# Performance work log

Hardware: AMD Instinct MI355X
Metric: run time of the kernel (lower is better)

Reference implementation:

```python
import jax, jax.numpy as jnp
import numpy as np
from math import sqrt

BATCH = 32
NUM_CLASSES = 81   # incl. background (class 0 skipped)
MAX_DET = 200      # max_output / per-class NMS candidate cap
IOU_T = 0.5        # criteria in decode_batch_with_nms_trace
CONF_T = 0.05      # score mask threshold


def make_dboxes():
    """Replicates dboxes_R34_coco([1200,1200]) -> (15130, 4) xywh, clipped to [0,1]."""
    fig = 1200
    feat = [50, 25, 13, 7, 3, 3]
    scales = [int(s * fig / 300) for s in [21, 45, 99, 153, 207, 261, 315]]
    ars = [[2], [2, 3], [2, 3], [2, 3], [2], [2]]
    boxes = []
    for idx, f in enumerate(feat):
        sk1 = scales[idx] / fig
        sk2 = scales[idx + 1] / fig
        sk3 = sqrt(sk1 * sk2)
        sizes = [(sk1, sk1), (sk3, sk3)]
        for a in ars[idx]:
            w, h = sk1 * sqrt(a), sk1 / sqrt(a)
            sizes += [(w, h), (h, w)]
        fk = fig // (fig // f)
        for (w, h) in sizes:
            for i in range(f):
                for j in range(f):
                    boxes.append(((j + 0.5) / fk, (i + 0.5) / fk, w, h))
    return np.clip(np.asarray(boxes, np.float32), 0.0, 1.0)


def setup_inputs() -> dict:
    key = jax.random.key(0)
    k1, k2 = jax.random.split(key)
    db = make_dboxes()                      # (15130, 4)
    N = db.shape[0]
    return {
        "bboxes_in": jax.random.normal(k1, (BATCH, 4, N), jnp.float32),
        "scores_in": jax.random.normal(k2, (BATCH, NUM_CLASSES, N), jnp.float32),
        "scale_xy": jnp.full((1,), 0.1, jnp.float32),
        "scale_wh": jnp.full((1,), 0.2, jnp.float32),
        "dboxes_xywh": jnp.asarray(db)[None],  # (1, N, 4)
    }


def _scale_back(bboxes_in, scores_in, scale_xy, scale_wh, dboxes_xywh):
    bb = jnp.transpose(bboxes_in, (0, 2, 1))          # (B, N, 4)
    sc = jnp.transpose(scores_in, (0, 2, 1))          # (B, N, L)
    d_xy, d_wh = dboxes_xywh[..., :2], dboxes_xywh[..., 2:]
    xy = bb[..., :2] * scale_xy * d_wh + d_xy
    wh = jnp.exp(bb[..., 2:] * scale_wh) * d_wh
    ltrb = jnp.concatenate([xy - 0.5 * wh, xy + 0.5 * wh], axis=-1)
    return ltrb, jax.nn.softmax(sc, axis=-1)


def _pairwise_iou(a, b):
    lt = jnp.maximum(a[:, None, :2], b[None, :, :2])
    rb = jnp.minimum(a[:, None, 2:], b[None, :, 2:])
    wh = jnp.clip(rb - lt, 0.0)
    inter = wh[..., 0] * wh[..., 1]
    area_a = (a[:, 2] - a[:, 0]) * (a[:, 3] - a[:, 1])
    area_b = (b[:, 2] - b[:, 0]) * (b[:, 3] - b[:, 1])
    return inter / (area_a[:, None] + area_b[None, :] - inter)


def _nms_one_class(boxes, cls_scores):
    """boxes (N,4), cls_scores (N,) -> (MAX_DET,4), (MAX_DET,) with suppressed = -1."""
    s = jnp.where(cls_scores > CONF_T, cls_scores, -1.0)   # mask score > 0.05
    top_s, idx = jax.lax.top_k(s, MAX_DET)                 # descending topk
    b = boxes[idx]
    iou = _pairwise_iou(b, b)                              # (K, K)
    valid = top_s > CONF_T

    def body(i, keep):  # greedy NMS over score-sorted candidates
        sup = (iou[i] > IOU_T) & keep[i] & (jnp.arange(MAX_DET) > i)
        return keep & ~sup

    keep = jax.lax.stop_gradient(jax.lax.fori_loop(0, MAX_DET, body, valid))
    return b, jnp.where(keep, top_s, -1.0)


def _decode(bboxes_in, scores_in, scale_xy, scale_wh, dboxes_xywh):
    boxes, probs = _scale_back(bboxes_in, scores_in, scale_xy, scale_wh, dboxes_xywh)
    cls_scores = jnp.transpose(probs[..., 1:], (0, 2, 1))   # (B, C=80, N); skip bg
    B, C = cls_scores.shape[0], cls_scores.shape[1]
    per_class = jax.vmap(_nms_one_class, in_axes=(None, 0))
    kb, ks = jax.vmap(per_class, in_axes=(0, 0))(boxes, cls_scores)  # (B,C,K,4),(B,C,K)
    labels = jnp.broadcast_to(
        jnp.arange(1, C + 1, dtype=jnp.int32)[:, None], (C, MAX_DET)).reshape(-1)
    kb = kb.reshape(B, C * MAX_DET, 4)
    ks = ks.reshape(B, C * MAX_DET)
    top_s, top_i = jax.lax.top_k(ks, MAX_DET)               # global top-200
    fb = jnp.take_along_axis(kb, top_i[..., None], axis=1)  # (B, 200, 4)
    fl = labels[top_i]                                      # (B, 200)
    valid = top_s > CONF_T
    return (fb * valid[..., None].astype(fb.dtype),
            jnp.where(valid, fl, 0),
            jnp.where(valid, top_s, 0.0))


def reference(bboxes_in, scores_in, scale_xy, scale_wh, dboxes_xywh):
    return _decode(bboxes_in, scores_in, scale_xy, scale_wh, dboxes_xywh)
```

## Files before the change

### kernel.cpp

```cpp
#include <hip/hip_runtime.h>
#include <stdint.h>

#define NPRIOR   15130
#define BATCH    32
#define NCLS     81
#define NCLS_OUT 80
#define NDET     200
#define CONF_T   0.05f
#define IOU_T    0.5f
#define CAND_CAP 1024
#define NGRP     5
#define GRP      16

__global__ __launch_bounds__(256) void zero_counters(unsigned int* __restrict__ counters, int n) {
    int i = blockIdx.x * 256 + threadIdx.x;
    if (i < n) counters[i] = 0u;
}

__global__ __launch_bounds__(256) void decode_softmax_scatter(
    const float* __restrict__ bboxes,
    const float* __restrict__ scores,
    const float* __restrict__ scale_xy_p,
    const float* __restrict__ scale_wh_p,
    const float* __restrict__ dboxes,
    float* __restrict__ boxes_ltrb,
    unsigned int* __restrict__ counters,
    unsigned long long* __restrict__ cand_g)
{
    int b = blockIdx.y;
    int n = blockIdx.x * 256 + threadIdx.x;
    if (n >= NPRIOR) return;

    float sx = scale_xy_p[0], sw = scale_wh_p[0];
    const float* bb = bboxes + (size_t)b * 4 * NPRIOR + n;
    float bx = bb[0];
    float by = bb[NPRIOR];
    float bw = bb[2 * NPRIOR];
    float bh = bb[3 * NPRIOR];
    float dx = dboxes[n * 4 + 0], dy = dboxes[n * 4 + 1];
    float dw = dboxes[n * 4 + 2], dh = dboxes[n * 4 + 3];
    float x = __fadd_rn(__fmul_rn(__fmul_rn(bx, sx), dw), dx);
    float y = __fadd_rn(__fmul_rn(__fmul_rn(by, sx), dh), dy);
    float w = __fmul_rn(expf(__fmul_rn(bw, sw)), dw);
    float h = __fmul_rn(expf(__fmul_rn(bh, sw)), dh);
    float hw = __fmul_rn(0.5f, w), hh = __fmul_rn(0.5f, h);
    float4 box;
    box.x = __fsub_rn(x, hw);
    box.y = __fsub_rn(y, hh);
    box.z = __fadd_rn(x, hw);
    box.w = __fadd_rn(y, hh);
    ((float4*)boxes_ltrb)[(size_t)b * NPRIOR + n] = box;

    const float* sc = scores + (size_t)b * NCLS * NPRIOR + n;
    float v[NCLS];
    float mx = -INFINITY;
#pragma unroll
    for (int c = 0; c < NCLS; ++c) {
        v[c] = sc[(size_t)c * NPRIOR];
        mx = fmaxf(mx, v[c]);
    }
    float sum = 0.f;
#pragma unroll
    for (int c = 0; c < NCLS; ++c) {
        v[c] = expf(__fsub_rn(v[c], mx));
        sum = __fadd_rn(sum, v[c]);
    }

    unsigned int invn = 0xFFFFFFFFu - (unsigned int)n;
#pragma unroll
    for (int c = 1; c < NCLS; ++c) {
        float p = __fdiv_rn(v[c], sum);
        if (p > CONF_T) {
            unsigned int idx = (unsigned int)b * NCLS_OUT + (unsigned int)(c - 1);
            unsigned int pos = atomicAdd(&counters[idx], 1u);
            if (pos < CAND_CAP) {
                cand_g[(size_t)idx * CAND_CAP + pos] =
                    ((unsigned long long)__float_as_uint(p) << 32) | (unsigned long long)invn;
            }
        }
    }
}

__device__ inline void bitonic_desc(unsigned long long* keys, int P, int tid) {
    for (int k = 2; k <= P; k <<= 1) {
        for (int j = k >> 1; j > 0; j >>= 1) {
            for (int i = tid; i < P; i += 256) {
                int l = i ^ j;
                if (l > i) {
                    unsigned long long a = keys[i], b = keys[l];
                    bool desc = ((i & k) == 0);
                    if (desc ? (a < b) : (a > b)) {
                        keys[i] = b;
                        keys[l] = a;
                    }
                }
            }
            __syncthreads();
        }
    }
}

__global__ __launch_bounds__(256) void nms_class(
    const unsigned int* __restrict__ counters,
    const unsigned long long* __restrict__ cand_g,
    const float* __restrict__ boxes_ltrb,
    float* __restrict__ cls_scores,
    float* __restrict__ cls_boxes)
{
    __shared__ unsigned long long cand[CAND_CAP];
    __shared__ float sbox[NDET][4];
    __shared__ float sscore[NDET];
    __shared__ unsigned long long rowm[NDET][4];
    __shared__ unsigned long long keepw[4];

    int tid = threadIdx.x;
    int b = blockIdx.y;
    int bc = b * NCLS_OUT + blockIdx.x;

    unsigned int cntu = counters[bc];
    int cnt = (cntu > CAND_CAP) ? CAND_CAP : (int)cntu;

    int P = 256;
    while (P < cnt) P <<= 1;

    for (int i = tid; i < P; i += 256)
        cand[i] = (i < cnt) ? cand_g[(size_t)bc * CAND_CAP + i] : 0ull;
    __syncthreads();

    bitonic_desc(cand, P, tid);

    int m = cnt < NDET ? cnt : NDET;
    if (tid < m) {
        unsigned long long key = cand[tid];
        unsigned int n = 0xFFFFFFFFu - (unsigned int)(key & 0xFFFFFFFFull);
        sscore[tid] = __uint_as_float((unsigned int)(key >> 32));
        float4 bx = ((const float4*)boxes_ltrb)[(size_t)b * NPRIOR + n];
        sbox[tid][0] = bx.x;
        sbox[tid][1] = bx.y;
        sbox[tid][2] = bx.z;
        sbox[tid][3] = bx.w;
    }
    __syncthreads();

    if (tid < m) {
        float l0 = sbox[tid][0], t0 = sbox[tid][1], r0 = sbox[tid][2], b0 = sbox[tid][3];
        float area0 = __fmul_rn(__fsub_rn(r0, l0), __fsub_rn(b0, t0));
        unsigned long long w0 = 0, w1 = 0, w2 = 0, w3 = 0;
        for (int j = tid + 1; j < m; ++j) {
            float lj = sbox[j][0], tj = sbox[j][1], rj = sbox[j][2], bj = sbox[j][3];
            float ltx = fmaxf(l0, lj), lty = fmaxf(t0, tj);
            float rbx = fminf(r0, rj), rby = fminf(b0, bj);
            float iw = fmaxf(__fsub_rn(rbx, ltx), 0.f);
            float ih = fmaxf(__fsub_rn(rby, lty), 0.f);
            float inter = __fmul_rn(iw, ih);
            float areaj = __fmul_rn(__fsub_rn(rj, lj), __fsub_rn(bj, tj));
            float den = __fsub_rn(__fadd_rn(area0, areaj), inter);
            float iou = __fdiv_rn(inter, den);
            if (iou > IOU_T) {
                if (j < 64) w0 |= 1ull << j;
                else if (j < 128) w1 |= 1ull << (j - 64);
                else if (j < 192) w2 |= 1ull << (j - 128);
                else w3 |= 1ull << (j - 192);
            }
        }
        rowm[tid][0] = w0;
        rowm[tid][1] = w1;
        rowm[tid][2] = w2;
        rowm[tid][3] = w3;
    }
    __syncthreads();

    if (tid == 0) {
        auto maskf = [](int t) -> unsigned long long {
            if (t <= 0) return 0ull;
            if (t >= 64) return ~0ull;
            return (1ull << t) - 1ull;
        };
        unsigned long long k0 = maskf(m), k1 = maskf(m - 64), k2 = maskf(m - 128), k3 = maskf(m - 192);
        for (int i = 0; i < m; ++i) {
            unsigned long long cur = (i < 64) ? k0 : (i < 128) ? k1 : (i < 192) ? k2 : k3;
            if ((cur >> (i & 63)) & 1ull) {
                k0 &= ~rowm[i][0];
                k1 &= ~rowm[i][1];
                k2 &= ~rowm[i][2];
                k3 &= ~rowm[i][3];
            }
        }
        keepw[0] = k0; keepw[1] = k1; keepw[2] = k2; keepw[3] = k3;
    }
    __syncthreads();

    if (tid < NDET) {
        float s = -1.0f;
        if (tid < m && ((keepw[tid >> 6] >> (tid & 63)) & 1ull)) s = sscore[tid];
        cls_scores[(size_t)bc * NDET + tid] = s;
        if (tid < m) {
            float4 bx;
            bx.x = sbox[tid][0]; bx.y = sbox[tid][1];
            bx.z = sbox[tid][2]; bx.w = sbox[tid][3];
            ((float4*)cls_boxes)[(size_t)bc * NDET + tid] = bx;
        }
    }
}

__global__ __launch_bounds__(256) void topk_group(
    const float* __restrict__ cls_scores,
    unsigned long long* __restrict__ grp_keys)
{
    __shared__ unsigned long long keys[4096];
    __shared__ unsigned int cnt_s;

    int tid = threadIdx.x;
    int g = blockIdx.x, b = blockIdx.y;
    if (tid == 0) cnt_s = 0;
    __syncthreads();

    int base_e = g * GRP * NDET;
    const float* sp = cls_scores + (size_t)b * NCLS_OUT * NDET + base_e;
    for (int i = tid; i < GRP * NDET; i += 256) {
        float s = sp[i];
        if (s > CONF_T) {
            unsigned int pos = atomicAdd(&cnt_s, 1u);
            unsigned int e = (unsigned int)(base_e + i);
            keys[pos] = ((unsigned long long)__float_as_uint(s) << 32) |
                        (unsigned long long)(0xFFFFFFFFu - e);
        }
    }
    __syncthreads();
    int cnt = (int)cnt_s;
    int P = 256;
    while (P < cnt) P <<= 1;
    for (int i = tid; i < P; i += 256)
        if (i >= cnt) keys[i] = 0ull;
    __syncthreads();

    bitonic_desc(keys, P, tid);

    if (tid < NDET)
        grp_keys[((size_t)b * NGRP + g) * NDET + tid] = (tid < cnt) ? keys[tid] : 0ull;
}

__global__ __launch_bounds__(256) void final_topk(
    const unsigned long long* __restrict__ grp_keys,
    const float* __restrict__ cls_boxes,
    float* __restrict__ out)
{
    __shared__ unsigned long long keys[1024];
    __shared__ unsigned int cnt_s;

    int tid = threadIdx.x, b = blockIdx.x;
    if (tid == 0) cnt_s = 0;
    __syncthreads();

    for (int i = tid; i < NGRP * NDET; i += 256) {
        unsigned long long k = grp_keys[(size_t)b * NGRP * NDET + i];
        if (k != 0ull) keys[atomicAdd(&cnt_s, 1u)] = k;
    }
    __syncthreads();
    int cnt = (int)cnt_s;
    int P = 256;
    while (P < cnt) P <<= 1;
    for (int i = tid; i < P; i += 256)
        if (i >= cnt) keys[i] = 0ull;
    __syncthreads();

    bitonic_desc(keys, P, tid);

    if (tid < NDET) {
        float4 bx = make_float4(0.f, 0.f, 0.f, 0.f);
        float lab = 0.f, sc = 0.f;
        if (tid < cnt) {
            unsigned long long k = keys[tid];
            unsigned int e = 0xFFFFFFFFu - (unsigned int)(k & 0xFFFFFFFFull);
            sc = __uint_as_float((unsigned int)(k >> 32));
            unsigned int c0 = e / NDET;
            bx = ((const float4*)cls_boxes)[(size_t)b * NCLS_OUT * NDET + e];
            lab = (float)(c0 + 1);
        }
        float* fb = out;
        float* fl = out + (size_t)BATCH * NDET * 4;
        float* fs = fl + (size_t)BATCH * NDET;
        ((float4*)fb)[b * NDET + tid] = bx;
        fl[b * NDET + tid] = lab;
        fs[b * NDET + tid] = sc;
    }
}

extern "C" void kernel_launch(void* const* d_in, const int* in_sizes, int n_in,
                              void* d_out, int out_size, void* d_ws, size_t ws_size,
                              hipStream_t stream) {
    const float* bboxes = (const float*)d_in[0];
    const float* scores = (const float*)d_in[1];
    const float* sxy    = (const float*)d_in[2];
    const float* swh    = (const float*)d_in[3];
    const float* dbx    = (const float*)d_in[4];
    float* out = (float*)d_out;

    char* ws = (char*)d_ws;
    size_t off = 0;
    auto alloc = [&](size_t bytes) -> char* {
        char* p = ws + off;
        off += (bytes + 255) & ~(size_t)255;
        return p;
    };
    float* boxes_ltrb            = (float*)alloc((size_t)BATCH * NPRIOR * 4 * 4);
    unsigned int* counters       = (unsigned int*)alloc((size_t)BATCH * NCLS_OUT * 4);
    unsigned long long* cand_g   = (unsigned long long*)alloc((size_t)BATCH * NCLS_OUT * CAND_CAP * 8);
    float* cls_scores            = (float*)alloc((size_t)BATCH * NCLS_OUT * NDET * 4);
    float* cls_boxes             = (float*)alloc((size_t)BATCH * NCLS_OUT * NDET * 4 * 4);
    unsigned long long* grp_keys = (unsigned long long*)alloc((size_t)BATCH * NGRP * NDET * 8);

    int ncounters = BATCH * NCLS_OUT;
    zero_counters<<<(ncounters + 255) / 256, 256, 0, stream>>>(counters, ncounters);

    dim3 gridA((NPRIOR + 255) / 256, BATCH);
    decode_softmax_scatter<<<gridA, 256, 0, stream>>>(
        bboxes, scores, sxy, swh, dbx, boxes_ltrb, counters, cand_g);

    dim3 gridB(NCLS_OUT, BATCH);
    nms_class<<<gridB, 256, 0, stream>>>(counters, cand_g, boxes_ltrb, cls_scores, cls_boxes);

    dim3 gridC1(NGRP, BATCH);
    topk_group<<<gridC1, 256, 0, stream>>>(cls_scores, grp_keys);

    final_topk<<<BATCH, 256, 0, stream>>>(grp_keys, cls_boxes, out);
}
```

Before: 799.0 us.

## Vectorize dbox load, memset counters, hoist NMS row loads, tweak launch bounds

```diff
diff --git a/kernel.cpp b/kernel.cpp
--- a/kernel.cpp
+++ b/kernel.cpp
@@ -11,13 +11,9 @@
 #define CAND_CAP 1024
 #define NGRP     5
 #define GRP      16
-
-__global__ __launch_bounds__(256) void zero_counters(unsigned int* __restrict__ counters, int n) {
-    int i = blockIdx.x * 256 + threadIdx.x;
-    if (i < n) counters[i] = 0u;
-}
-
-__global__ __launch_bounds__(256) void decode_softmax_scatter(
+#define NCNT     (BATCH * NCLS_OUT)
+
+__global__ __launch_bounds__(256, 1) void decode_softmax_scatter(
     const float* __restrict__ bboxes,
     const float* __restrict__ scores,
     const float* __restrict__ scale_xy_p,
@@ -37,12 +33,11 @@
     float by = bb[NPRIOR];
     float bw = bb[2 * NPRIOR];
     float bh = bb[3 * NPRIOR];
-    float dx = dboxes[n * 4 + 0], dy = dboxes[n * 4 + 1];
-    float dw = dboxes[n * 4 + 2], dh = dboxes[n * 4 + 3];
-    float x = __fadd_rn(__fmul_rn(__fmul_rn(bx, sx), dw), dx);
-    float y = __fadd_rn(__fmul_rn(__fmul_rn(by, sx), dh), dy);
-    float w = __fmul_rn(expf(__fmul_rn(bw, sw)), dw);
-    float h = __fmul_rn(expf(__fmul_rn(bh, sw)), dh);
+    float4 d = ((const float4*)dboxes)[n];
+    float x = __fadd_rn(__fmul_rn(__fmul_rn(bx, sx), d.z), d.x);
+    float y = __fadd_rn(__fmul_rn(__fmul_rn(by, sx), d.w), d.y);
+    float w = __fmul_rn(expf(__fmul_rn(bw, sw)), d.z);
+    float h = __fmul_rn(expf(__fmul_rn(bh, sw)), d.w);
     float hw = __fmul_rn(0.5f, w), hh = __fmul_rn(0.5f, h);
     float4 box;
     box.x = __fsub_rn(x, hw);
@@ -67,11 +62,12 @@
     }
 
     unsigned int invn = 0xFFFFFFFFu - (unsigned int)n;
+    unsigned int cbase = (unsigned int)b * NCLS_OUT;
 #pragma unroll
     for (int c = 1; c < NCLS; ++c) {
         float p = __fdiv_rn(v[c], sum);
         if (p > CONF_T) {
-            unsigned int idx = (unsigned int)b * NCLS_OUT + (unsigned int)(c - 1);
+            unsigned int idx = cbase + (unsigned int)(c - 1);
             unsigned int pos = atomicAdd(&counters[idx], 1u);
             if (pos < CAND_CAP) {
                 cand_g[(size_t)idx * CAND_CAP + pos] =
@@ -177,13 +173,13 @@
             return (1ull << t) - 1ull;
         };
         unsigned long long k0 = maskf(m), k1 = maskf(m - 64), k2 = maskf(m - 128), k3 = maskf(m - 192);
+#pragma unroll 4
         for (int i = 0; i < m; ++i) {
+            unsigned long long r0 = rowm[i][0], r1 = rowm[i][1];
+            unsigned long long r2 = rowm[i][2], r3 = rowm[i][3];
             unsigned long long cur = (i < 64) ? k0 : (i < 128) ? k1 : (i < 192) ? k2 : k3;
             if ((cur >> (i & 63)) & 1ull) {
-                k0 &= ~rowm[i][0];
-                k1 &= ~rowm[i][1];
-                k2 &= ~rowm[i][2];
-                k3 &= ~rowm[i][3];
+                k0 &= ~r0; k1 &= ~r1; k2 &= ~r2; k3 &= ~r3;
             }
         }
         keepw[0] = k0; keepw[1] = k1; keepw[2] = k2; keepw[3] = k3;
@@ -304,14 +300,13 @@
         return p;
     };
     float* boxes_ltrb            = (float*)alloc((size_t)BATCH * NPRIOR * 4 * 4);
-    unsigned int* counters       = (unsigned int*)alloc((size_t)BATCH * NCLS_OUT * 4);
-    unsigned long long* cand_g   = (unsigned long long*)alloc((size_t)BATCH * NCLS_OUT * CAND_CAP * 8);
+    unsigned int* counters       = (unsigned int*)alloc((size_t)NCNT * 4);
+    unsigned long long* cand_g   = (unsigned long long*)alloc((size_t)NCNT * CAND_CAP * 8);
     float* cls_scores            = (float*)alloc((size_t)BATCH * NCLS_OUT * NDET * 4);
     float* cls_boxes             = (float*)alloc((size_t)BATCH * NCLS_OUT * NDET * 4 * 4);
     unsigned long long* grp_keys = (unsigned long long*)alloc((size_t)BATCH * NGRP * NDET * 8);
 
-    int ncounters = BATCH * NCLS_OUT;
-    zero_counters<<<(ncounters + 255) / 256, 256, 0, stream>>>(counters, ncounters);
+    hipMemsetAsync(counters, 0, (size_t)NCNT * 4, stream);
 
     dim3 gridA((NPRIOR + 255) / 256, BATCH);
     decode_softmax_scatter<<<gridA, 256, 0, stream>>>(
```

After: 812.9 us. About the same (+1.7%).
